# Kernel tuning notes

Measured on AMD Instinct MI355X. Metric: run time of the kernel, lower is better.

The kernel has to match this reference:

```python
import jax, jax.numpy as jnp
import numpy as np

WINDOW = 128
LOOK_BACK = 1
LOOK_FWD = 0   # causal=True -> look_forward defaults to 0
DIM = 64       # rotary dim == head dim


def look_around(x, backward=LOOK_BACK, forward=LOOK_FWD, pad_value=-1):
    # x: [b, windows, window, ...]; pad along windows axis, concat along axis 2
    w = x.shape[1]
    pad = [(0, 0), (backward, forward)] + [(0, 0)] * (x.ndim - 2)
    px = jnp.pad(x, pad, constant_values=pad_value)
    return jnp.concatenate([px[:, i:i + w] for i in range(forward + backward + 1)], axis=2)


def rotate_half(x):
    h = (x.shape[-1] + 1) // 2  # ceil split, matches torch .split([ceil, floor])
    x1, x2 = x[..., :h], x[..., h:]
    return jnp.concatenate([-x2, x1], axis=-1)


def setup_inputs() -> dict:
    key = jax.random.key(0)
    kq, kk, kv = jax.random.split(key, 3)
    shape = (4, 16, 4096, 64)
    return {
        "q": jax.random.normal(kq, shape, dtype=jnp.float32),
        "k": jax.random.normal(kk, shape, dtype=jnp.float32),
        "v": jax.random.normal(kv, shape, dtype=jnp.float32),
    }


def reference(q, k, v):
    B, H, T, e = q.shape
    b = B * H
    q, k, v = (t.reshape(b, T, e) for t in (q, k, v))

    # sinusoidal rotary embeddings (start_pos = 0)
    inv_freq = 1.0 / (10000.0 ** (jnp.arange(0, DIM, 2, dtype=jnp.float32) / DIM))
    t_idx = jnp.arange(T, dtype=jnp.float32)
    freqs = jnp.einsum('i,j->ij', t_idx, inv_freq)          # [T, DIM/2]
    emb = jnp.concatenate([freqs, freqs], axis=-1)[:, :DIM][None]  # [1, T, DIM]
    cos, sin = jnp.cos(emb), jnp.sin(emb)
    q = q * cos + rotate_half(q) * sin
    k = k * cos + rotate_half(k) * sin

    # T is a multiple of WINDOW so autopad is a no-op
    w = T // WINDOW
    bq, bk, bv = (t.reshape(b, w, WINDOW, e) for t in (q, k, v))
    bk = look_around(bk)   # [b, w, (LB+LF+1)*WINDOW, e], padded with -1 (masked below)
    bv = look_around(bv)

    b_t = jnp.arange(T).reshape(1, w, WINDOW)
    bq_t = b_t
    bq_k = look_around(b_t)  # [1, w, (LB+LF+1)*WINDOW]

    dots = (jnp.einsum('bwie,bwje->bwij', bq.astype(jnp.float32), bk.astype(jnp.float32))
            * (e ** -0.5)).astype(q.dtype)
    mask_value = -jnp.finfo(dots.dtype).max

    # causal mask (exact_windowsize=False)
    causal_mask = bq_t[:, :, :, None] < bq_k[:, :, None, :]
    dots = jnp.where(causal_mask, mask_value, dots)
    # look-around padding mask
    dots = jnp.where((bq_k == -1)[:, :, None, :], mask_value, dots)

    attn = jax.nn.softmax(dots, axis=-1)
    out = jnp.einsum('bwij,bwje->bwie', attn, bv)
    return out.reshape(B, H, T, e)
```

## Files before the change

### kernel.cpp

```cpp
#include <hip/hip_runtime.h>

#define T_LEN 4096
#define DHEAD 64
#define WINSZ 128
#define KVLEN 256
#define NWIN 32
#define NBH 64
#define FLTMAX 3.402823466e38f

typedef float f32x4 __attribute__((ext_vector_type(4)));
typedef short s16x8 __attribute__((ext_vector_type(8)));
typedef short s16x4 __attribute__((ext_vector_type(4)));

__device__ __forceinline__ unsigned short f2b(float x) {
  unsigned u = __builtin_bit_cast(unsigned, x);
  u += 0x7fffu + ((u >> 16) & 1u);
  return (unsigned short)(u >> 16);
}

__global__ void rope_tab_kernel(float* __restrict__ tab) {
  const int idx = blockIdx.x * 256 + threadIdx.x;
  if (idx >= T_LEN * 32) return;
  const int t = idx >> 5;
  const int i = idx & 31;
  const float freq = powf(10000.0f, -(float)i / 32.0f);
  float s, c;
  sincosf((float)t * freq, &s, &c);
  tab[idx] = c;
  tab[T_LEN * 32 + idx] = s;
}

__global__ __launch_bounds__(256, 2) void lattn_kernel(
    const float* __restrict__ qg, const float* __restrict__ kg,
    const float* __restrict__ vg, const float* __restrict__ tab,
    float* __restrict__ outg) {
  __shared__ __align__(16) unsigned short Kl[KVLEN * DHEAD];
  __shared__ __align__(16) unsigned short Vt[DHEAD * KVLEN];

  const int bid = blockIdx.x;
  const int win = bid & (NWIN - 1);
  const int bh  = bid >> 5;
  const int tid = threadIdx.x;
  const int lane = tid & 63;
  const int wv = tid >> 6;
  const int l15 = lane & 15;
  const int g = lane >> 4;

  const size_t base = (size_t)bh * T_LEN * DHEAD;
  const int q0 = win * WINSZ;
  const int k0 = q0 - WINSZ;
  const bool use_tab = (tab != nullptr);
  const float* ct = tab;
  const float* st = tab + T_LEN * 32;

  {
    const int c = tid & 7;
    const int rr = tid >> 3;
    float fr[4];
    if (!use_tab) {
      #pragma unroll
      for (int j = 0; j < 4; ++j)
        fr[j] = powf(10000.0f, -(float)(4 * c + j) / 32.0f);
    }
    #pragma unroll
    for (int p = 0; p < 8; ++p) {
      const int kr = p * 32 + rr;
      const int kt = k0 + kr;
      float xa[4] = {0.f,0.f,0.f,0.f}, xb[4] = {0.f,0.f,0.f,0.f};
      float cs[4], sn[4];
      #pragma unroll
      for (int j = 0; j < 4; ++j) { cs[j] = 1.f; sn[j] = 0.f; }
      if (kt >= 0) {
        const float* kp = kg + base + (size_t)kt * DHEAD + 4 * c;
        *(float4*)xa = *(const float4*)kp;
        *(float4*)xb = *(const float4*)(kp + 32);
        if (use_tab) {
          *(float4*)cs = *(const float4*)(ct + kt * 32 + 4 * c);
          *(float4*)sn = *(const float4*)(st + kt * 32 + 4 * c);
        } else {
          #pragma unroll
          for (int j = 0; j < 4; ++j) sincosf((float)kt * fr[j], &sn[j], &cs[j]);
        }
      }
      unsigned wlo[2], whi[2];
      #pragma unroll
      for (int h = 0; h < 2; ++h) {
        const int j0 = 2 * h, j1 = 2 * h + 1;
        wlo[h] = (unsigned)f2b(xa[j0]*cs[j0] - xb[j0]*sn[j0]) |
                 ((unsigned)f2b(xa[j1]*cs[j1] - xb[j1]*sn[j1]) << 16);
        whi[h] = (unsigned)f2b(xb[j0]*cs[j0] + xa[j0]*sn[j0]) |
                 ((unsigned)f2b(xb[j1]*cs[j1] + xa[j1]*sn[j1]) << 16);
      }
      const int su = (kr & 7) << 3;
      uint2 a = {wlo[0], wlo[1]}, b = {whi[0], whi[1]};
      *(uint2*)&Kl[kr * 64 + ((4 * c) ^ su)] = a;
      *(uint2*)&Kl[kr * 64 + ((4 * c + 32) ^ su)] = b;
    }
  }

  {
    const int c = tid & 15;
    const int rp = tid >> 4;
    #pragma unroll
    for (int p = 0; p < 8; ++p) {
      const int kr = (p * 16 + rp) * 2;
      const int kt = k0 + kr;
      float va[4] = {0.f,0.f,0.f,0.f}, vb[4] = {0.f,0.f,0.f,0.f};
      if (kt >= 0)
        *(float4*)va = *(const float4*)(vg + base + (size_t)kt * DHEAD + 4 * c);
      if (kt + 1 >= 0)
        *(float4*)vb = *(const float4*)(vg + base + (size_t)(kt + 1) * DHEAD + 4 * c);
      #pragma unroll
      for (int j = 0; j < 4; ++j) {
        const int d = 4 * c + j;
        const unsigned val = (unsigned)f2b(va[j]) | ((unsigned)f2b(vb[j]) << 16);
        *(unsigned*)&Vt[d * 256 + (kr ^ ((d & 7) << 3))] = val;
      }
    }
  }

  s16x8 qa[2][2];
  {
    float fr[8];
    if (!use_tab) {
      #pragma unroll
      for (int j = 0; j < 8; ++j)
        fr[j] = powf(10000.0f, -(float)(8 * g + j) / 32.0f);
    }
    #pragma unroll
    for (int mtl = 0; mtl < 2; ++mtl) {
      const int qrow = q0 + wv * 32 + mtl * 16 + l15;
      const float* qp = qg + base + (size_t)qrow * DHEAD + 8 * g;
      float xa[8], xb[8], cs[8], sn[8];
      *(float4*)&xa[0] = *(const float4*)qp;
      *(float4*)&xa[4] = *(const float4*)(qp + 4);
      *(float4*)&xb[0] = *(const float4*)(qp + 32);
      *(float4*)&xb[4] = *(const float4*)(qp + 36);
      if (use_tab) {
        const float* cp = ct + qrow * 32 + 8 * g;
        const float* sp = st + qrow * 32 + 8 * g;
        *(float4*)&cs[0] = *(const float4*)cp;
        *(float4*)&cs[4] = *(const float4*)(cp + 4);
        *(float4*)&sn[0] = *(const float4*)sp;
        *(float4*)&sn[4] = *(const float4*)(sp + 4);
      } else {
        #pragma unroll
        for (int j = 0; j < 8; ++j) sincosf((float)qrow * fr[j], &sn[j], &cs[j]);
      }
      #pragma unroll
      for (int j = 0; j < 8; ++j) {
        qa[mtl][0][j] = (short)f2b(xa[j]*cs[j] - xb[j]*sn[j]);
        qa[mtl][1][j] = (short)f2b(xb[j]*cs[j] + xa[j]*sn[j]);
      }
    }
  }

  __syncthreads();

  s16x8 pa[2][8];
  #pragma unroll
  for (int mtl = 0; mtl < 2; ++mtl) {
    f32x4 acc[16];
    #pragma unroll
    for (int nt = 0; nt < 16; ++nt) acc[nt] = f32x4{0.f, 0.f, 0.f, 0.f};
    #pragma unroll
    for (int nt = 0; nt < 16; ++nt) {
      const int krow = nt * 16 + l15;
      const int su = (krow & 7) << 3;
      const s16x8 k0f = *(const s16x8*)&Kl[krow * 64 + ((8 * g) ^ su)];
      const s16x8 k1f = *(const s16x8*)&Kl[krow * 64 + ((8 * g + 32) ^ su)];
      acc[nt] = __builtin_amdgcn_mfma_f32_16x16x32_bf16(k0f, qa[mtl][0], acc[nt], 0, 0, 0);
      acc[nt] = __builtin_amdgcn_mfma_f32_16x16x32_bf16(k1f, qa[mtl][1], acc[nt], 0, 0, 0);
    }
    const int qloc = wv * 32 + mtl * 16 + l15;
    float mx = -FLTMAX;
    #pragma unroll
    for (int nt = 0; nt < 16; ++nt) {
      const bool pad = (win == 0) && (nt < 8);
      #pragma unroll
      for (int r = 0; r < 4; ++r) {
        const int kloc = nt * 16 + 4 * g + r;
        const bool msk = pad || (kloc > WINSZ + qloc);
        const float s = msk ? -FLTMAX : acc[nt][r];
        acc[nt][r] = s;
        mx = fmaxf(mx, s);
      }
    }
    mx = fmaxf(mx, __shfl_xor(mx, 16));
    mx = fmaxf(mx, __shfl_xor(mx, 32));
    float den = 0.f;
    #pragma unroll
    for (int nt = 0; nt < 16; ++nt) {
      #pragma unroll
      for (int r = 0; r < 4; ++r) {
        const float pv = __expf(0.125f * (acc[nt][r] - mx));
        acc[nt][r] = pv;
        den += pv;
      }
    }
    den += __shfl_xor(den, 16);
    den += __shfl_xor(den, 32);
    const float inv = 1.0f / den;
    #pragma unroll
    for (int ks = 0; ks < 8; ++ks) {
      #pragma unroll
      for (int j = 0; j < 4; ++j) {
        pa[mtl][ks][j]     = (short)f2b(acc[2 * ks][j] * inv);
        pa[mtl][ks][j + 4] = (short)f2b(acc[2 * ks + 1][j] * inv);
      }
    }
  }

  f32x4 oacc[2][4];
  #pragma unroll
  for (int mtl = 0; mtl < 2; ++mtl)
    #pragma unroll
    for (int nt = 0; nt < 4; ++nt) oacc[mtl][nt] = f32x4{0.f, 0.f, 0.f, 0.f};

  #pragma unroll
  for (int ks = 0; ks < 8; ++ks) {
    #pragma unroll
    for (int nt = 0; nt < 4; ++nt) {
      const int d = nt * 16 + l15;
      const int su = (d & 7) << 3;
      const int c1 = ks * 32 + 4 * g;
      const s16x4 v0 = *(const s16x4*)&Vt[d * 256 + (c1 ^ su)];
      const s16x4 v1 = *(const s16x4*)&Vt[d * 256 + ((c1 + 16) ^ su)];
      const s16x8 vb = __builtin_shufflevector(v0, v1, 0, 1, 2, 3, 4, 5, 6, 7);
      oacc[0][nt] = __builtin_amdgcn_mfma_f32_16x16x32_bf16(pa[0][ks], vb, oacc[0][nt], 0, 0, 0);
      oacc[1][nt] = __builtin_amdgcn_mfma_f32_16x16x32_bf16(pa[1][ks], vb, oacc[1][nt], 0, 0, 0);
    }
  }

  float* op = outg + base;
  #pragma unroll
  for (int mtl = 0; mtl < 2; ++mtl) {
    #pragma unroll
    for (int r = 0; r < 4; ++r) {
      const int qrow = q0 + wv * 32 + mtl * 16 + 4 * g + r;
      #pragma unroll
      for (int nt = 0; nt < 4; ++nt)
        op[(size_t)qrow * DHEAD + nt * 16 + l15] = oacc[mtl][nt][r];
    }
  }
}

extern "C" void kernel_launch(void* const* d_in, const int* in_sizes, int n_in,
                              void* d_out, int out_size, void* d_ws, size_t ws_size,
                              hipStream_t stream) {
  (void)in_sizes; (void)n_in; (void)out_size;
  const float* q = (const float*)d_in[0];
  const float* k = (const float*)d_in[1];
  const float* v = (const float*)d_in[2];
  float* out = (float*)d_out;

  float* tab = nullptr;
  const size_t tab_bytes = (size_t)2 * T_LEN * 32 * sizeof(float);
  if (ws_size >= tab_bytes) {
    tab = (float*)d_ws;
    rope_tab_kernel<<<dim3((T_LEN * 32 + 255) / 256), dim3(256), 0, stream>>>(tab);
  }
  lattn_kernel<<<dim3(NBH * NWIN), dim3(256), 0, stream>>>(q, k, v, tab, out);
}
```

Measured before the change: 242.1 us.

## Use 512-thread blocks with one 16-row query tile per wave

Doubles the threads per block from 256 to 512 so each of the 8 waves handles a single 16-row query tile instead of two. The cooperative K/V staging loops are halved to match. This is meant to raise wave-level parallelism and lower per-thread register pressure (launch bounds now target 4 blocks of 512). Each K/V LDS fragment is now reused by fewer query tiles per wave, so total LDS reads per block rise.

After: 227.3 us. 6.1% less time.

```diff
diff --git a/kernel.cpp b/kernel.cpp
--- a/kernel.cpp
+++ b/kernel.cpp
@@ -30,7 +30,7 @@
   tab[T_LEN * 32 + idx] = s;
 }
 
-__global__ __launch_bounds__(256, 2) void lattn_kernel(
+__global__ __launch_bounds__(512, 4) void lattn_kernel(
     const float* __restrict__ qg, const float* __restrict__ kg,
     const float* __restrict__ vg, const float* __restrict__ tab,
     float* __restrict__ outg) {
@@ -63,8 +63,8 @@
         fr[j] = powf(10000.0f, -(float)(4 * c + j) / 32.0f);
     }
     #pragma unroll
-    for (int p = 0; p < 8; ++p) {
-      const int kr = p * 32 + rr;
+    for (int p = 0; p < 4; ++p) {
+      const int kr = p * 64 + rr;
       const int kt = k0 + kr;
       float xa[4] = {0.f,0.f,0.f,0.f}, xb[4] = {0.f,0.f,0.f,0.f};
       float cs[4], sn[4];
@@ -102,8 +102,8 @@
     const int c = tid & 15;
     const int rp = tid >> 4;
     #pragma unroll
-    for (int p = 0; p < 8; ++p) {
-      const int kr = (p * 16 + rp) * 2;
+    for (int p = 0; p < 4; ++p) {
+      const int kr = (p * 32 + rp) * 2;
       const int kt = k0 + kr;
       float va[4] = {0.f,0.f,0.f,0.f}, vb[4] = {0.f,0.f,0.f,0.f};
       if (kt >= 0)
@@ -119,47 +119,40 @@
     }
   }
 
-  s16x8 qa[2][2];
-  {
-    float fr[8];
-    if (!use_tab) {
-      #pragma unroll
-      for (int j = 0; j < 8; ++j)
-        fr[j] = powf(10000.0f, -(float)(8 * g + j) / 32.0f);
-    }
-    #pragma unroll
-    for (int mtl = 0; mtl < 2; ++mtl) {
-      const int qrow = q0 + wv * 32 + mtl * 16 + l15;
-      const float* qp = qg + base + (size_t)qrow * DHEAD + 8 * g;
-      float xa[8], xb[8], cs[8], sn[8];
-      *(float4*)&xa[0] = *(const float4*)qp;
-      *(float4*)&xa[4] = *(const float4*)(qp + 4);
-      *(float4*)&xb[0] = *(const float4*)(qp + 32);
-      *(float4*)&xb[4] = *(const float4*)(qp + 36);
-      if (use_tab) {
-        const float* cp = ct + qrow * 32 + 8 * g;
-        const float* sp = st + qrow * 32 + 8 * g;
-        *(float4*)&cs[0] = *(const float4*)cp;
-        *(float4*)&cs[4] = *(const float4*)(cp + 4);
-        *(float4*)&sn[0] = *(const float4*)sp;
-        *(float4*)&sn[4] = *(const float4*)(sp + 4);
-      } else {
-        #pragma unroll
-        for (int j = 0; j < 8; ++j) sincosf((float)qrow * fr[j], &sn[j], &cs[j]);
-      }
+  s16x8 qa[2];
+  {
+    const int qrow = q0 + wv * 16 + l15;
+    const float* qp = qg + base + (size_t)qrow * DHEAD + 8 * g;
+    float xa[8], xb[8], cs[8], sn[8];
+    *(float4*)&xa[0] = *(const float4*)qp;
+    *(float4*)&xa[4] = *(const float4*)(qp + 4);
+    *(float4*)&xb[0] = *(const float4*)(qp + 32);
+    *(float4*)&xb[4] = *(const float4*)(qp + 36);
+    if (use_tab) {
+      const float* cp = ct + qrow * 32 + 8 * g;
+      const float* sp = st + qrow * 32 + 8 * g;
+      *(float4*)&cs[0] = *(const float4*)cp;
+      *(float4*)&cs[4] = *(const float4*)(cp + 4);
+      *(float4*)&sn[0] = *(const float4*)sp;
+      *(float4*)&sn[4] = *(const float4*)(sp + 4);
+    } else {
       #pragma unroll
       for (int j = 0; j < 8; ++j) {
-        qa[mtl][0][j] = (short)f2b(xa[j]*cs[j] - xb[j]*sn[j]);
-        qa[mtl][1][j] = (short)f2b(xb[j]*cs[j] + xa[j]*sn[j]);
-      }
+        const float f = powf(10000.0f, -(float)(8 * g + j) / 32.0f);
+        sincosf((float)qrow * f, &sn[j], &cs[j]);
+      }
+    }
+    #pragma unroll
+    for (int j = 0; j < 8; ++j) {
+      qa[0][j] = (short)f2b(xa[j]*cs[j] - xb[j]*sn[j]);
+      qa[1][j] = (short)f2b(xb[j]*cs[j] + xa[j]*sn[j]);
     }
   }
 
   __syncthreads();
 
-  s16x8 pa[2][8];
-  #pragma unroll
-  for (int mtl = 0; mtl < 2; ++mtl) {
+  s16x8 pa[8];
+  {
     f32x4 acc[16];
     #pragma unroll
     for (int nt = 0; nt < 16; ++nt) acc[nt] = f32x4{0.f, 0.f, 0.f, 0.f};
@@ -169,10 +162,10 @@
       const int su = (krow & 7) << 3;
       const s16x8 k0f = *(const s16x8*)&Kl[krow * 64 + ((8 * g) ^ su)];
       const s16x8 k1f = *(const s16x8*)&Kl[krow * 64 + ((8 * g + 32) ^ su)];
-      acc[nt] = __builtin_amdgcn_mfma_f32_16x16x32_bf16(k0f, qa[mtl][0], acc[nt], 0, 0, 0);
-      acc[nt] = __builtin_amdgcn_mfma_f32_16x16x32_bf16(k1f, qa[mtl][1], acc[nt], 0, 0, 0);
-    }
-    const int qloc = wv * 32 + mtl * 16 + l15;
+      acc[nt] = __builtin_amdgcn_mfma_f32_16x16x32_bf16(k0f, qa[0], acc[nt], 0, 0, 0);
+      acc[nt] = __builtin_amdgcn_mfma_f32_16x16x32_bf16(k1f, qa[1], acc[nt], 0, 0, 0);
+    }
+    const int qloc = wv * 16 + l15;
     float mx = -FLTMAX;
     #pragma unroll
     for (int nt = 0; nt < 16; ++nt) {
@@ -205,17 +198,15 @@
     for (int ks = 0; ks < 8; ++ks) {
       #pragma unroll
       for (int j = 0; j < 4; ++j) {
-        pa[mtl][ks][j]     = (short)f2b(acc[2 * ks][j] * inv);
-        pa[mtl][ks][j + 4] = (short)f2b(acc[2 * ks + 1][j] * inv);
-      }
-    }
-  }
-
-  f32x4 oacc[2][4];
+        pa[ks][j]     = (short)f2b(acc[2 * ks][j] * inv);
+        pa[ks][j + 4] = (short)f2b(acc[2 * ks + 1][j] * inv);
+      }
+    }
+  }
+
+  f32x4 oacc[4];
   #pragma unroll
-  for (int mtl = 0; mtl < 2; ++mtl)
-    #pragma unroll
-    for (int nt = 0; nt < 4; ++nt) oacc[mtl][nt] = f32x4{0.f, 0.f, 0.f, 0.f};
+  for (int nt = 0; nt < 4; ++nt) oacc[nt] = f32x4{0.f, 0.f, 0.f, 0.f};
 
   #pragma unroll
   for (int ks = 0; ks < 8; ++ks) {
@@ -227,21 +218,17 @@
       const s16x4 v0 = *(const s16x4*)&Vt[d * 256 + (c1 ^ su)];
       const s16x4 v1 = *(const s16x4*)&Vt[d * 256 + ((c1 + 16) ^ su)];
       const s16x8 vb = __builtin_shufflevector(v0, v1, 0, 1, 2, 3, 4, 5, 6, 7);
-      oacc[0][nt] = __builtin_amdgcn_mfma_f32_16x16x32_bf16(pa[0][ks], vb, oacc[0][nt], 0, 0, 0);
-      oacc[1][nt] = __builtin_amdgcn_mfma_f32_16x16x32_bf16(pa[1][ks], vb, oacc[1][nt], 0, 0, 0);
+      oacc[nt] = __builtin_amdgcn_mfma_f32_16x16x32_bf16(pa[ks], vb, oacc[nt], 0, 0, 0);
     }
   }
 
   float* op = outg + base;
   #pragma unroll
-  for (int mtl = 0; mtl < 2; ++mtl) {
-    #pragma unroll
-    for (int r = 0; r < 4; ++r) {
-      const int qrow = q0 + wv * 32 + mtl * 16 + 4 * g + r;
-      #pragma unroll
-      for (int nt = 0; nt < 4; ++nt)
-        op[(size_t)qrow * DHEAD + nt * 16 + l15] = oacc[mtl][nt][r];
-    }
+  for (int r = 0; r < 4; ++r) {
+    const int qrow = q0 + wv * 16 + 4 * g + r;
+    #pragma unroll
+    for (int nt = 0; nt < 4; ++nt)
+      op[(size_t)qrow * DHEAD + nt * 16 + l15] = oacc[nt][r];
   }
 }
 
@@ -260,5 +247,5 @@
     tab = (float*)d_ws;
     rope_tab_kernel<<<dim3((T_LEN * 32 + 255) / 256), dim3(256), 0, stream>>>(tab);
   }
-  lattn_kernel<<<dim3(NBH * NWIN), dim3(256), 0, stream>>>(q, k, v, tab, out);
-}
+  lattn_kernel<<<dim3(NBH * NWIN), dim3(512), 0, stream>>>(q, k, v, tab, out);
+}
```
